# Performance work log

Measured on AMD Instinct MI355X. Metric: run time of the kernel, lower is better.

## Reference

```python
import jax, jax.numpy as jnp
import numpy as np

D_MODEL = 1024
NUM_HEAD = 16
D_K = D_MODEL // NUM_HEAD


def setup_inputs() -> dict:
    key = jax.random.key(0)
    ks = jax.random.split(key, 9)
    s = 1.0 / np.sqrt(D_MODEL)
    x = jax.random.normal(ks[0], (2, 2048, D_MODEL), dtype=jnp.float32)
    Wq = jax.random.uniform(ks[1], (D_MODEL, D_MODEL), jnp.float32, -s, s)
    bq = jax.random.uniform(ks[2], (D_MODEL,), jnp.float32, -s, s)
    Wk = jax.random.uniform(ks[3], (D_MODEL, D_MODEL), jnp.float32, -s, s)
    bk = jax.random.uniform(ks[4], (D_MODEL,), jnp.float32, -s, s)
    Wv = jax.random.uniform(ks[5], (D_MODEL, D_MODEL), jnp.float32, -s, s)
    bv = jax.random.uniform(ks[6], (D_MODEL,), jnp.float32, -s, s)
    Wo = jax.random.uniform(ks[7], (D_MODEL, D_MODEL), jnp.float32, -s, s)
    bo = jax.random.uniform(ks[8], (D_MODEL,), jnp.float32, -s, s)
    return {"x": x, "Wq": Wq, "bq": bq, "Wk": Wk, "bk": bk,
            "Wv": Wv, "bv": bv, "Wo": Wo, "bo": bo}


def reference(x, Wq, bq, Wk, bk, Wv, bv, Wo, bo):
    b, n, d = x.shape
    h, dk = NUM_HEAD, D_K
    # Linear projections (torch Linear: x @ W.T + b)
    q = (x @ Wq.T + bq).reshape(b, n, h, dk).transpose(0, 2, 1, 3)  # [b,h,n,dk]
    k = (x @ Wk.T + bk).reshape(b, n, h, dk).transpose(0, 2, 1, 3)
    v = (x @ Wv.T + bv).reshape(b, n, h, dk).transpose(0, 2, 1, 3)
    scores = jnp.einsum('bhqd,bhkd->bhqk', q, k) / jnp.sqrt(jnp.float32(dk))
    attn = jax.nn.softmax(scores, axis=-1)  # [b,h,n,n]
    out = jnp.einsum('bhqk,bhkd->bhqd', attn, v)
    out = out.transpose(0, 2, 1, 3).reshape(b, n, d)
    return out @ Wo.T + bo
```

## Files before the change

### kernel.cpp

```cpp
#include <hip/hip_runtime.h>

#define BATCH   2
#define SEQ     2048
#define DMODEL  1024
#define NHEAD   16
#define DKH     64
#define MTOT    (BATCH*SEQ)
#define KDIM    DMODEL

#define XB    0u
#define WQB   (4u*1024u*1024u)
#define WKB   (5u*1024u*1024u)
#define WVB   (6u*1024u*1024u)
#define WOB   (7u*1024u*1024u)
#define QOFF  (8u*1024u*1024u)
#define KOFF  (12u*1024u*1024u)
#define VOFF  (16u*1024u*1024u)
#define OOFF  (20u*1024u*1024u)

typedef __bf16 bf16x8 __attribute__((ext_vector_type(8)));
typedef __bf16 bf16x4 __attribute__((ext_vector_type(4)));
typedef float  f32x4  __attribute__((ext_vector_type(4)));
typedef float  f32x16 __attribute__((ext_vector_type(16)));

__device__ __forceinline__ void async16(const __bf16* g, __bf16* l) {
  __builtin_amdgcn_global_load_lds(
      (const __attribute__((address_space(1))) void*)g,
      (__attribute__((address_space(3))) void*)l, 16, 0, 0);
}

#define VWAIT(N) asm volatile("s_waitcnt vmcnt(" #N ")" ::: "memory")

__device__ __forceinline__ unsigned cvtpk_bf16(float lo, float hi) {
  unsigned r;
  asm("v_cvt_pk_bf16_f32 %0, %1, %2" : "=v"(r) : "v"(lo), "v"(hi));
  return r;
}
__device__ __forceinline__ void plswap(unsigned& a, unsigned& b) {
  asm("v_permlane32_swap_b32 %0, %1" : "+v"(a), "+v"(b));
}

__global__ __launch_bounds__(256) void cvt_fp32_bf16(
    const float* __restrict__ x,  const float* __restrict__ wq,
    const float* __restrict__ wk, const float* __restrict__ wv,
    const float* __restrict__ wo, __bf16* __restrict__ ws)
{
  const float* src; __bf16* dst; int n;
  switch (blockIdx.y) {
    case 0:  src = x;  dst = ws + XB;  n = 4 * 1024 * 1024; break;
    case 1:  src = wq; dst = ws + WQB; n = 1024 * 1024;     break;
    case 2:  src = wk; dst = ws + WKB; n = 1024 * 1024;     break;
    case 3:  src = wv; dst = ws + WVB; n = 1024 * 1024;     break;
    default: src = wo; dst = ws + WOB; n = 1024 * 1024;     break;
  }
  const int i = (blockIdx.x * 256 + threadIdx.x) * 8;
  if (i < n) {
    const float4 a = *(const float4*)(src + i);
    const float4 b = *(const float4*)(src + i + 4);
    bf16x8 o;
    o[0] = (__bf16)a.x; o[1] = (__bf16)a.y; o[2] = (__bf16)a.z; o[3] = (__bf16)a.w;
    o[4] = (__bf16)b.x; o[5] = (__bf16)b.y; o[6] = (__bf16)b.z; o[7] = (__bf16)b.w;
    *(bf16x8*)(dst + i) = o;
  }
}

__device__ __forceinline__ void gemm_stage128(
    const __bf16* __restrict__ A, const __bf16* __restrict__ W,
    int m0, int n0, int kt, __bf16* slot, int w, int lane)
{
#pragma unroll
  for (int issue = 0; issue < 2; ++issue) {
    const int cbase = issue * 256 + (w << 6);
    const int c     = cbase + lane;
    const int row   = c >> 2;
    const int goff  = ((c & 3) ^ (row & 3)) << 3;
    async16(A + (size_t)(m0 + row) * KDIM + kt + goff, slot + cbase * 8);
    async16(W + (size_t)(n0 + row) * KDIM + kt + goff, slot + 4096 + cbase * 8);
  }
}

__device__ __forceinline__ void gemm_step128(
    const __bf16* slot, int wr, int wc, int ln15, int quad, f32x4 (&acc)[4][4])
{
  const __bf16* A_lds = slot;
  const __bf16* B_lds = slot + 4096;
  bf16x8 af[4], bfr[4];
#pragma unroll
  for (int i = 0; i < 4; ++i) {
    const int row = wr + i * 16 + ln15;
    af[i] = *(const bf16x8*)&A_lds[row * 32 + ((quad ^ (row & 3)) << 3)];
  }
#pragma unroll
  for (int j = 0; j < 4; ++j) {
    const int row = wc + j * 16 + ln15;
    bfr[j] = *(const bf16x8*)&B_lds[row * 32 + ((quad ^ (row & 3)) << 3)];
  }
#pragma unroll
  for (int i = 0; i < 4; ++i)
#pragma unroll
    for (int j = 0; j < 4; ++j)
      acc[i][j] = __builtin_amdgcn_mfma_f32_16x16x32_bf16(af[i], bfr[j], acc[i][j], 0, 0, 0);
}

__device__ __forceinline__ void gemm128_core(
    const __bf16* __restrict__ A, const __bf16* __restrict__ W,
    int m0, int n0, __bf16* lds, f32x4 (&acc)[4][4])
{
  const int t    = threadIdx.x;
  const int w    = t >> 6;
  const int lane = t & 63;
  const int ln15 = lane & 15;
  const int quad = lane >> 4;
  const int wr   = (w >> 1) << 6;
  const int wc   = (w & 1) << 6;

#pragma unroll
  for (int i = 0; i < 4; ++i)
#pragma unroll
    for (int j = 0; j < 4; ++j) acc[i][j] = (f32x4){0.f, 0.f, 0.f, 0.f};

  __bf16* s0 = lds;
  __bf16* s1 = lds + 8192;
  __bf16* s2 = lds + 16384;

  gemm_stage128(A, W, m0, n0, 0,  s0, w, lane);
  gemm_stage128(A, W, m0, n0, 32, s1, w, lane);

  int kt = 0;
#pragma unroll 1
  for (int i3 = 0; i3 < 10; ++i3) {
    VWAIT(4); __builtin_amdgcn_s_barrier();
    gemm_stage128(A, W, m0, n0, kt + 64, s2, w, lane);
    gemm_step128(s0, wr, wc, ln15, quad, acc);

    VWAIT(4); __builtin_amdgcn_s_barrier();
    gemm_stage128(A, W, m0, n0, kt + 96, s0, w, lane);
    gemm_step128(s1, wr, wc, ln15, quad, acc);

    VWAIT(4); __builtin_amdgcn_s_barrier();
    gemm_stage128(A, W, m0, n0, kt + 128, s1, w, lane);
    gemm_step128(s2, wr, wc, ln15, quad, acc);
    kt += 96;
  }
  VWAIT(4); __builtin_amdgcn_s_barrier();
  gemm_step128(s0, wr, wc, ln15, quad, acc);
  VWAIT(0); __builtin_amdgcn_s_barrier();
  gemm_step128(s1, wr, wc, ln15, quad, acc);
}

__global__ __launch_bounds__(256) void qkv_gemm(
    const __bf16* __restrict__ X,
    const __bf16* __restrict__ Wq, const float* __restrict__ bq,
    const __bf16* __restrict__ Wk, const float* __restrict__ bk,
    const __bf16* __restrict__ Wv, const float* __restrict__ bv,
    __bf16* __restrict__ ws)
{
  __shared__ __align__(16) __bf16 lds[24576];

  const int z = blockIdx.z;
  const __bf16* W    = (z == 0) ? Wq : (z == 1) ? Wk : Wv;
  const float*  bias = (z == 0) ? bq : (z == 1) ? bk : bv;
  __bf16* out = ws + ((z == 0) ? QOFF : (z == 1) ? KOFF : VOFF);
  const float scale = (z == 0) ? 0.125f * 1.44269504088896f : 1.0f;

  const int m0 = blockIdx.x * 128;
  const int n0 = blockIdx.y * 128;

  f32x4 acc[4][4];
  gemm128_core(X, W, m0, n0, lds, acc);

  const int t = threadIdx.x, w = t >> 6, lane = t & 63;
  const int ln15 = lane & 15, quad = lane >> 4;
  const int wr = (w >> 1) << 6, wc = (w & 1) << 6;

  float bj4[4];
#pragma unroll
  for (int j = 0; j < 4; ++j) bj4[j] = bias[n0 + wc + j * 16 + ln15];

  __syncthreads();
  __bf16* scr = lds + (w << 10);

  const int bb = m0 >> 11;
  const int s_base = (m0 & 2047) + wr;
  const int h = (n0 + wc) >> 6;

  if (z != 2) {
    const int rdrow = lane & 15, rdseg = lane >> 4;
#pragma unroll
    for (int i = 0; i < 4; ++i) {
#pragma unroll
      for (int j = 0; j < 4; ++j)
#pragma unroll
        for (int rr = 0; rr < 4; ++rr)
          scr[(quad * 4 + rr) * 64 + j * 16 + ln15] =
              (__bf16)((acc[i][j][rr] + bj4[j]) * scale);
      bf16x8 v0 = *(const bf16x8*)&scr[rdrow * 64 + rdseg * 16];
      bf16x8 v1 = *(const bf16x8*)&scr[rdrow * 64 + rdseg * 16 + 8];
      const int s = s_base + i * 16 + rdrow;
      __bf16* p = out + (((size_t)(bb * NHEAD + h)) * SEQ + s) * DKH + rdseg * 16;
      *(bf16x8*)p = v0;
      *(bf16x8*)&p[8] = v1;
    }
  } else {
#pragma unroll
    for (int i = 0; i < 4; ++i) {
#pragma unroll
      for (int j = 0; j < 4; ++j) {
        bf16x4 pk;
#pragma unroll
        for (int rr = 0; rr < 4; ++rr) pk[rr] = (__bf16)(acc[i][j][rr] + bj4[j]);
        *(bf16x4*)&scr[(j * 16 + ln15) * 16 + quad * 4] = pk;
      }
      bf16x8 c0 = *(const bf16x8*)&scr[lane * 16];
      bf16x8 c1 = *(const bf16x8*)&scr[lane * 16 + 8];
      __bf16* p = out + (((size_t)(bb * NHEAD + h)) * DKH + lane) * SEQ
                      + s_base + i * 16;
      *(bf16x8*)p = c0;
      *(bf16x8*)&p[8] = c1;
    }
  }
}

__device__ __forceinline__ void out_stage(
    const __bf16* __restrict__ A, const __bf16* __restrict__ Wo,
    int m0, int n0, int kt, __bf16* slot, int w, int lane)
{
  {
    const int c = (w << 6) + lane;
    const int row = c >> 2;
    const int goff = ((c & 3) ^ (row & 3)) << 3;
    async16(A + (size_t)(m0 + row) * KDIM + kt + goff, slot + c * 8);
  }
#pragma unroll
  for (int issue = 0; issue < 2; ++issue) {
    const int cbase = issue * 256 + (w << 6);
    const int c = cbase + lane;
    const int row = c >> 2;
    const int goff = ((c & 3) ^ (row & 3)) << 3;
    async16(Wo + (size_t)(n0 + row) * KDIM + kt + goff, slot + 2048 + cbase * 8);
  }
}

__device__ __forceinline__ void out_step(
    const __bf16* slot, int w, int ln15, int quad, f32x4 (&acc)[4][2])
{
  const __bf16* A_lds = slot;
  const __bf16* B_lds = slot + 2048;
  bf16x8 af[4], bfr[2];
#pragma unroll
  for (int i = 0; i < 4; ++i) {
    const int row = i * 16 + ln15;
    af[i] = *(const bf16x8*)&A_lds[row * 32 + ((quad ^ (row & 3)) << 3)];
  }
#pragma unroll
  for (int j = 0; j < 2; ++j) {
    const int row = (w << 5) + j * 16 + ln15;
    bfr[j] = *(const bf16x8*)&B_lds[row * 32 + ((quad ^ (row & 3)) << 3)];
  }
#pragma unroll
  for (int i = 0; i < 4; ++i)
#pragma unroll
    for (int j = 0; j < 2; ++j)
      acc[i][j] = __builtin_amdgcn_mfma_f32_16x16x32_bf16(af[i], bfr[j], acc[i][j], 0, 0, 0);
}

__global__ __launch_bounds__(256) void out_gemm(
    const __bf16* __restrict__ A, const __bf16* __restrict__ Wo,
    const float* __restrict__ bo, float* __restrict__ out)
{
  __shared__ __align__(16) __bf16 lds[18432];

  const int m0 = blockIdx.x * 64;
  const int n0 = blockIdx.y * 128;

  const int t = threadIdx.x, w = t >> 6, lane = t & 63;
  const int ln15 = lane & 15, quad = lane >> 4;

  f32x4 acc[4][2];
#pragma unroll
  for (int i = 0; i < 4; ++i)
#pragma unroll
    for (int j = 0; j < 2; ++j) acc[i][j] = (f32x4){0.f, 0.f, 0.f, 0.f};

  __bf16* s0 = lds;
  __bf16* s1 = lds + 6144;
  __bf16* s2 = lds + 12288;

  out_stage(A, Wo, m0, n0, 0,  s0, w, lane);
  out_stage(A, Wo, m0, n0, 32, s1, w, lane);

  int kt = 0;
#pragma unroll 1
  for (int i3 = 0; i3 < 10; ++i3) {
    VWAIT(3); __builtin_amdgcn_s_barrier();
    out_stage(A, Wo, m0, n0, kt + 64, s2, w, lane);
    out_step(s0, w, ln15, quad, acc);

    VWAIT(3); __builtin_amdgcn_s_barrier();
    out_stage(A, Wo, m0, n0, kt + 96, s0, w, lane);
    out_step(s1, w, ln15, quad, acc);

    VWAIT(3); __builtin_amdgcn_s_barrier();
    out_stage(A, Wo, m0, n0, kt + 128, s1, w, lane);
    out_step(s2, w, ln15, quad, acc);
    kt += 96;
  }
  VWAIT(3); __builtin_amdgcn_s_barrier();
  out_step(s0, w, ln15, quad, acc);
  VWAIT(0); __builtin_amdgcn_s_barrier();
  out_step(s1, w, ln15, quad, acc);

  float bj2[2];
#pragma unroll
  for (int j = 0; j < 2; ++j) bj2[j] = bo[n0 + (w << 5) + j * 16 + ln15];

  __syncthreads();
  float* scrf = (float*)lds + (w << 9);

  const int rdrow = lane & 15, rdseg = lane >> 4;
#pragma unroll
  for (int i = 0; i < 4; ++i) {
#pragma unroll
    for (int j = 0; j < 2; ++j) {
      f32x4 v;
#pragma unroll
      for (int rr = 0; rr < 4; ++rr) v[rr] = acc[i][j][rr] + bj2[j];
      *(f32x4*)&scrf[(j * 16 + ln15) * 16 + quad * 4] = v;
    }
    const int m = m0 + i * 16 + rdrow;
    float* p = out + (size_t)m * DMODEL + n0 + (w << 5) + rdseg * 8;
#pragma unroll
    for (int cc = 0; cc < 2; ++cc) {
      f32x4 v;
#pragma unroll
      for (int e = 0; e < 4; ++e)
        v[e] = scrf[(rdseg * 8 + cc * 4 + e) * 16 + rdrow];
      *(f32x4*)&p[cc * 4] = v;
    }
  }
}

__device__ __forceinline__ void softmax_frag(const f32x16& s, float& l,
                                             bf16x8& pfa, bf16x8& pfb)
{
  float p[16];
#pragma unroll
  for (int r = 0; r < 16; ++r) {
    p[r] = __builtin_amdgcn_exp2f(s[r]);
    l += p[r];
  }
  unsigned A0 = cvtpk_bf16(p[0],  p[1]);
  unsigned A1 = cvtpk_bf16(p[2],  p[3]);
  unsigned B0 = cvtpk_bf16(p[4],  p[5]);
  unsigned B1 = cvtpk_bf16(p[6],  p[7]);
  unsigned C0 = cvtpk_bf16(p[8],  p[9]);
  unsigned C1 = cvtpk_bf16(p[10], p[11]);
  unsigned D0 = cvtpk_bf16(p[12], p[13]);
  unsigned D1 = cvtpk_bf16(p[14], p[15]);
  plswap(A0, B0);
  plswap(A1, B1);
  plswap(C0, D0);
  plswap(C1, D1);
  union { unsigned u[4]; bf16x8 v; } ua, ub;
  ua.u[0] = A0; ua.u[1] = A1; ua.u[2] = B0; ua.u[3] = B1;
  ub.u[0] = C0; ub.u[1] = C1; ub.u[2] = D0; ub.u[3] = D1;
  pfa = ua.v;
  pfb = ub.v;
}

__device__ __forceinline__ void pvstep(const __bf16* Vs, int kh, int KS, int hl,
                                       int ln31, const bf16x8& PF,
                                       f32x16& o0, f32x16& o1)
{
  const int vchunk = (kh << 3) + 2 * KS + hl;
  bf16x8 vf0 = *(const bf16x8*)&Vs[ln31 * 128 + ((vchunk ^ (ln31 & 15)) << 3)];
  bf16x8 vf1 = *(const bf16x8*)&Vs[(32 + ln31) * 128 +
                                   ((vchunk ^ ((32 + ln31) & 15)) << 3)];
  o0 = __builtin_amdgcn_mfma_f32_32x32x16_bf16(PF, vf0, o0, 0, 0, 0);
  o1 = __builtin_amdgcn_mfma_f32_32x32x16_bf16(PF, vf1, o1, 0, 0, 0);
}

__device__ __forceinline__ void attn_tile_compute(
    const __bf16* Ks, const __bf16* Vs, const bf16x8 (&qf)[4],
    int kh, int ln31, int hl, float& l_lane, f32x16& o0, f32x16& o1)
{
#pragma unroll
  for (int half = 0; half < 2; ++half) {
    f32x16 s;
#pragma unroll
    for (int r = 0; r < 16; ++r) s[r] = 0.f;
    const int kr = (kh << 6) + half * 32 + ln31;
    __builtin_amdgcn_s_setprio(1);
#pragma unroll
    for (int ks = 0; ks < 4; ++ks) {
      bf16x8 kf = *(const bf16x8*)&Ks[kr * 64 + (((2 * ks + hl) ^ (kr & 7)) << 3)];
      s = __builtin_amdgcn_mfma_f32_32x32x16_bf16(kf, qf[ks], s, 0, 0, 0);
    }
    __builtin_amdgcn_s_setprio(0);
    bf16x8 pa, pb;
    softmax_frag(s, l_lane, pa, pb);
    __builtin_amdgcn_s_setprio(1);
    pvstep(Vs, kh, half * 2 + 0, hl, ln31, pa, o0, o1);
    pvstep(Vs, kh, half * 2 + 1, hl, ln31, pb, o0, o1);
    __builtin_amdgcn_s_setprio(0);
  }
}

__global__ __launch_bounds__(512, 4) void attn_kernel(
    const __bf16* __restrict__ Qb, const __bf16* __restrict__ Kb,
    const __bf16* __restrict__ Vtb, __bf16* __restrict__ Ob)
{
  __shared__ __align__(16) __bf16 smem[5 * 128 * 64];
  __bf16* QP = smem;
  __bf16* K0 = smem + 8192;
  __bf16* V0 = smem + 16384;
  __bf16* K1 = smem + 24576;
  __bf16* V1 = smem + 32768;

  const int t = threadIdx.x, w = t >> 6, lane = t & 63;
  const int ln31 = lane & 31, hl = lane >> 5;
  const int g  = w & 3;
  const int kh = w >> 2;
  const int bh = blockIdx.x;
  const int q0 = blockIdx.y * 128;
  const int bb = bh >> 4, hh = bh & 15;

  const __bf16* Qg = Qb + (size_t)bh * SEQ * DKH + (size_t)q0 * DKH;
  const __bf16* Kg = Kb + (size_t)bh * SEQ * DKH;
  const __bf16* Vg = Vtb + (size_t)bh * DKH * SEQ;

  auto stage_kv = [&](int kt, __bf16* Ks, __bf16* Vs) {
#pragma unroll
    for (int issue = 0; issue < 2; ++issue) {
      const int cbase = issue * 512 + (w << 6);
      const int c = cbase + lane;
      const int krow = c >> 3;
      const int kgoff = ((c & 7) ^ (krow & 7)) << 3;
      async16(Kg + (size_t)(kt + krow) * DKH + kgoff, Ks + cbase * 8);
      const int vrow = c >> 4;
      const int vgoff = ((c & 15) ^ (vrow & 15)) << 3;
      async16(Vg + (size_t)vrow * SEQ + kt + vgoff, Vs + cbase * 8);
    }
  };

#pragma unroll
  for (int issue = 0; issue < 2; ++issue) {
    const int cbase = issue * 512 + (w << 6);
    const int c = cbase + lane;
    const int row = c >> 3;
    const int goff = ((c & 7) ^ (row & 7)) << 3;
    async16(Qg + (size_t)row * DKH + goff, QP + cbase * 8);
  }
  stage_kv(0, K0, V0);
  stage_kv(128, K1, V1);

  VWAIT(8);
  __builtin_amdgcn_s_barrier();

  const int qrow = (g << 5) + ln31;
  bf16x8 qf[4];
#pragma unroll
  for (int ks = 0; ks < 4; ++ks) {
    const int chunk = ((2 * ks + hl) ^ (qrow & 7));
    qf[ks] = *(const bf16x8*)&QP[qrow * 64 + (chunk << 3)];
  }

  float l_lane = 0.f;
  f32x16 o0, o1;
#pragma unroll
  for (int r = 0; r < 16; ++r) { o0[r] = 0.f; o1[r] = 0.f; }

#pragma unroll 1
  for (int j = 0; j < 14; j += 2) {
    VWAIT(4); __builtin_amdgcn_s_barrier();
    attn_tile_compute(K0, V0, qf, kh, ln31, hl, l_lane, o0, o1);
    __builtin_amdgcn_s_barrier();
    stage_kv((j + 2) * 128, K0, V0);

    VWAIT(4); __builtin_amdgcn_s_barrier();
    attn_tile_compute(K1, V1, qf, kh, ln31, hl, l_lane, o0, o1);
    __builtin_amdgcn_s_barrier();
    stage_kv((j + 3) * 128, K1, V1);
  }
  VWAIT(4); __builtin_amdgcn_s_barrier();
  attn_tile_compute(K0, V0, qf, kh, ln31, hl, l_lane, o0, o1);
  VWAIT(0); __builtin_amdgcn_s_barrier();
  attn_tile_compute(K1, V1, qf, kh, ln31, hl, l_lane, o0, o1);

  __syncthreads();
  float* cmb = (float*)smem;
  const int dsw = ln31 & 7;
  l_lane += __shfl_xor(l_lane, 32);

  if (w >= 4) {
    float* base = cmb + (g << 11);
#pragma unroll
    for (int gg = 0; gg < 4; ++gg) {
      const int qq = ((2 * gg + hl) ^ dsw) << 2;
      f32x4 va, vb;
#pragma unroll
      for (int rr = 0; rr < 4; ++rr) { va[rr] = o0[4 * gg + rr]; vb[rr] = o1[4 * gg + rr]; }
      *(f32x4*)&base[ln31 * 32 + qq]        = va;
      *(f32x4*)&base[(32 + ln31) * 32 + qq] = vb;
    }
    if (hl == 0) cmb[8192 + (g << 5) + ln31] = l_lane;
  }
  __syncthreads();
  if (w < 4) {
    float* base = cmb + (g << 11);
#pragma unroll
    for (int gg = 0; gg < 4; ++gg) {
      const int qq = ((2 * gg + hl) ^ dsw) << 2;
      const f32x4 va = *(const f32x4*)&base[ln31 * 32 + qq];
      const f32x4 vb = *(const f32x4*)&base[(32 + ln31) * 32 + qq];
#pragma unroll
      for (int rr = 0; rr < 4; ++rr) { o0[4 * gg + rr] += va[rr]; o1[4 * gg + rr] += vb[rr]; }
    }
    const float inv = 1.0f / (l_lane + cmb[8192 + (g << 5) + ln31]);

#pragma unroll
    for (int r = 0; r < 16; ++r) {
      const int qi = (r & 3) + 8 * (r >> 2) + 4 * hl;
      const float iq = __shfl(inv, qi);
      const int q = q0 + (g << 5) + qi;
      __bf16* rowp = Ob + ((size_t)(bb * SEQ + q)) * DMODEL + hh * DKH;
      rowp[ln31]      = (__bf16)(o0[r] * iq);
      rowp[32 + ln31] = (__bf16)(o1[r] * iq);
    }
  }
}

extern "C" void kernel_launch(void* const* d_in, const int* in_sizes, int n_in,
                              void* d_out, int out_size, void* d_ws, size_t ws_size,
                              hipStream_t stream)
{
  const float* x  = (const float*)d_in[0];
  const float* Wq = (const float*)d_in[1];
  const float* bq = (const float*)d_in[2];
  const float* Wk = (const float*)d_in[3];
  const float* bk = (const float*)d_in[4];
  const float* Wv = (const float*)d_in[5];
  const float* bv = (const float*)d_in[6];
  const float* Wo = (const float*)d_in[7];
  const float* bo = (const float*)d_in[8];
  float*  out = (float*)d_out;
  __bf16* ws  = (__bf16*)d_ws;

  cvt_fp32_bf16<<<dim3(2048, 5, 1), 256, 0, stream>>>(x, Wq, Wk, Wv, Wo, ws);

  qkv_gemm<<<dim3(MTOT / 128, DMODEL / 128, 3), 256, 0, stream>>>(
      ws + XB, ws + WQB, bq, ws + WKB, bk, ws + WVB, bv, ws);

  attn_kernel<<<dim3(BATCH * NHEAD, SEQ / 128), 512, 0, stream>>>(
      ws + QOFF, ws + KOFF, ws + VOFF, ws + OOFF);

  out_gemm<<<dim3(MTOT / 64, DMODEL / 128), 256, 0, stream>>>(
      ws + OOFF, ws + WOB, bo, out);
}
```

Before: 182.9 us.

## Split QKV GEMM 128x128 tile across 8 waves instead of 4

The QKV projection kernel now launches 512 threads per block, with each wave computing a 64x32 sub-tile instead of 64x64. Staging loads are spread over all threads with one async load per operand, and the epilogue writes narrower per-wave slices. The aim is more waves per CU to hide memory and MFMA latency, at the cost of lower register-level reuse per wave and more barrier participants.

Result: no change. 180.6 us (median of 2 runs) (-1.3%).

```diff
diff --git a/kernel.cpp b/kernel.cpp
--- a/kernel.cpp
+++ b/kernel.cpp
@@ -64,91 +64,41 @@
   }
 }
 
-__device__ __forceinline__ void gemm_stage128(
+__device__ __forceinline__ void qkv_stage(
     const __bf16* __restrict__ A, const __bf16* __restrict__ W,
-    int m0, int n0, int kt, __bf16* slot, int w, int lane)
-{
-#pragma unroll
-  for (int issue = 0; issue < 2; ++issue) {
-    const int cbase = issue * 256 + (w << 6);
-    const int c     = cbase + lane;
-    const int row   = c >> 2;
-    const int goff  = ((c & 3) ^ (row & 3)) << 3;
-    async16(A + (size_t)(m0 + row) * KDIM + kt + goff, slot + cbase * 8);
-    async16(W + (size_t)(n0 + row) * KDIM + kt + goff, slot + 4096 + cbase * 8);
-  }
-}
-
-__device__ __forceinline__ void gemm_step128(
-    const __bf16* slot, int wr, int wc, int ln15, int quad, f32x4 (&acc)[4][4])
+    int m0, int n0, int kt, __bf16* slot, int t)
+{
+  const int c    = t;
+  const int row  = c >> 2;
+  const int goff = ((c & 3) ^ (row & 3)) << 3;
+  async16(A + (size_t)(m0 + row) * KDIM + kt + goff, slot + c * 8);
+  async16(W + (size_t)(n0 + row) * KDIM + kt + goff, slot + 4096 + c * 8);
+}
+
+__device__ __forceinline__ void qkv_step(
+    const __bf16* slot, int wr, int wc, int ln15, int quad, f32x4 (&acc)[4][2])
 {
   const __bf16* A_lds = slot;
   const __bf16* B_lds = slot + 4096;
-  bf16x8 af[4], bfr[4];
+  bf16x8 af[4], bfr[2];
 #pragma unroll
   for (int i = 0; i < 4; ++i) {
     const int row = wr + i * 16 + ln15;
     af[i] = *(const bf16x8*)&A_lds[row * 32 + ((quad ^ (row & 3)) << 3)];
   }
 #pragma unroll
-  for (int j = 0; j < 4; ++j) {
+  for (int j = 0; j < 2; ++j) {
     const int row = wc + j * 16 + ln15;
     bfr[j] = *(const bf16x8*)&B_lds[row * 32 + ((quad ^ (row & 3)) << 3)];
   }
 #pragma unroll
   for (int i = 0; i < 4; ++i)
 #pragma unroll
-    for (int j = 0; j < 4; ++j)
+    for (int j = 0; j < 2; ++j)
       acc[i][j] = __builtin_amdgcn_mfma_f32_16x16x32_bf16(af[i], bfr[j], acc[i][j], 0, 0, 0);
 }
 
-__device__ __forceinline__ void gemm128_core(
-    const __bf16* __restrict__ A, const __bf16* __restrict__ W,
-    int m0, int n0, __bf16* lds, f32x4 (&acc)[4][4])
-{
-  const int t    = threadIdx.x;
-  const int w    = t >> 6;
-  const int lane = t & 63;
-  const int ln15 = lane & 15;
-  const int quad = lane >> 4;
-  const int wr   = (w >> 1) << 6;
-  const int wc   = (w & 1) << 6;
-
-#pragma unroll
-  for (int i = 0; i < 4; ++i)
-#pragma unroll
-    for (int j = 0; j < 4; ++j) acc[i][j] = (f32x4){0.f, 0.f, 0.f, 0.f};
-
-  __bf16* s0 = lds;
-  __bf16* s1 = lds + 8192;
-  __bf16* s2 = lds + 16384;
-
-  gemm_stage128(A, W, m0, n0, 0,  s0, w, lane);
-  gemm_stage128(A, W, m0, n0, 32, s1, w, lane);
-
-  int kt = 0;
-#pragma unroll 1
-  for (int i3 = 0; i3 < 10; ++i3) {
-    VWAIT(4); __builtin_amdgcn_s_barrier();
-    gemm_stage128(A, W, m0, n0, kt + 64, s2, w, lane);
-    gemm_step128(s0, wr, wc, ln15, quad, acc);
-
-    VWAIT(4); __builtin_amdgcn_s_barrier();
-    gemm_stage128(A, W, m0, n0, kt + 96, s0, w, lane);
-    gemm_step128(s1, wr, wc, ln15, quad, acc);
-
-    VWAIT(4); __builtin_amdgcn_s_barrier();
-    gemm_stage128(A, W, m0, n0, kt + 128, s1, w, lane);
-    gemm_step128(s2, wr, wc, ln15, quad, acc);
-    kt += 96;
-  }
-  VWAIT(4); __builtin_amdgcn_s_barrier();
-  gemm_step128(s0, wr, wc, ln15, quad, acc);
-  VWAIT(0); __builtin_amdgcn_s_barrier();
-  gemm_step128(s1, wr, wc, ln15, quad, acc);
-}
-
-__global__ __launch_bounds__(256) void qkv_gemm(
+__global__ __launch_bounds__(512, 3) void qkv_gemm(
     const __bf16* __restrict__ X,
     const __bf16* __restrict__ Wq, const float* __restrict__ bq,
     const __bf16* __restrict__ Wk, const float* __restrict__ bk,
@@ -166,16 +116,48 @@
   const int m0 = blockIdx.x * 128;
   const int n0 = blockIdx.y * 128;
 
-  f32x4 acc[4][4];
-  gemm128_core(X, W, m0, n0, lds, acc);
-
   const int t = threadIdx.x, w = t >> 6, lane = t & 63;
   const int ln15 = lane & 15, quad = lane >> 4;
-  const int wr = (w >> 1) << 6, wc = (w & 1) << 6;
-
-  float bj4[4];
-#pragma unroll
-  for (int j = 0; j < 4; ++j) bj4[j] = bias[n0 + wc + j * 16 + ln15];
+  const int wr = (w >> 2) << 6;
+  const int wc = (w & 3) << 5;
+
+  f32x4 acc[4][2];
+#pragma unroll
+  for (int i = 0; i < 4; ++i)
+#pragma unroll
+    for (int j = 0; j < 2; ++j) acc[i][j] = (f32x4){0.f, 0.f, 0.f, 0.f};
+
+  __bf16* s0 = lds;
+  __bf16* s1 = lds + 8192;
+  __bf16* s2 = lds + 16384;
+
+  qkv_stage(X, W, m0, n0, 0,  s0, t);
+  qkv_stage(X, W, m0, n0, 32, s1, t);
+
+  int kt = 0;
+#pragma unroll 1
+  for (int i3 = 0; i3 < 10; ++i3) {
+    VWAIT(2); __builtin_amdgcn_s_barrier();
+    qkv_stage(X, W, m0, n0, kt + 64, s2, t);
+    qkv_step(s0, wr, wc, ln15, quad, acc);
+
+    VWAIT(2); __builtin_amdgcn_s_barrier();
+    qkv_stage(X, W, m0, n0, kt + 96, s0, t);
+    qkv_step(s1, wr, wc, ln15, quad, acc);
+
+    VWAIT(2); __builtin_amdgcn_s_barrier();
+    qkv_stage(X, W, m0, n0, kt + 128, s1, t);
+    qkv_step(s2, wr, wc, ln15, quad, acc);
+    kt += 96;
+  }
+  VWAIT(2); __builtin_amdgcn_s_barrier();
+  qkv_step(s0, wr, wc, ln15, quad, acc);
+  VWAIT(0); __builtin_amdgcn_s_barrier();
+  qkv_step(s1, wr, wc, ln15, quad, acc);
+
+  float bj2[2];
+#pragma unroll
+  for (int j = 0; j < 2; ++j) bj2[j] = bias[n0 + wc + j * 16 + ln15];
 
   __syncthreads();
   __bf16* scr = lds + (w << 10);
@@ -189,34 +171,32 @@
 #pragma unroll
     for (int i = 0; i < 4; ++i) {
 #pragma unroll
-      for (int j = 0; j < 4; ++j)
+      for (int j = 0; j < 2; ++j)
 #pragma unroll
         for (int rr = 0; rr < 4; ++rr)
-          scr[(quad * 4 + rr) * 64 + j * 16 + ln15] =
-              (__bf16)((acc[i][j][rr] + bj4[j]) * scale);
-      bf16x8 v0 = *(const bf16x8*)&scr[rdrow * 64 + rdseg * 16];
-      bf16x8 v1 = *(const bf16x8*)&scr[rdrow * 64 + rdseg * 16 + 8];
+          scr[(quad * 4 + rr) * 32 + j * 16 + ln15] =
+              (__bf16)((acc[i][j][rr] + bj2[j]) * scale);
+      bf16x8 v = *(const bf16x8*)&scr[rdrow * 32 + rdseg * 8];
       const int s = s_base + i * 16 + rdrow;
-      __bf16* p = out + (((size_t)(bb * NHEAD + h)) * SEQ + s) * DKH + rdseg * 16;
-      *(bf16x8*)p = v0;
-      *(bf16x8*)&p[8] = v1;
+      __bf16* p = out + (((size_t)(bb * NHEAD + h)) * SEQ + s) * DKH
+                      + (wc & 63) + rdseg * 8;
+      *(bf16x8*)p = v;
     }
   } else {
 #pragma unroll
     for (int i = 0; i < 4; ++i) {
 #pragma unroll
-      for (int j = 0; j < 4; ++j) {
+      for (int j = 0; j < 2; ++j) {
         bf16x4 pk;
 #pragma unroll
-        for (int rr = 0; rr < 4; ++rr) pk[rr] = (__bf16)(acc[i][j][rr] + bj4[j]);
+        for (int rr = 0; rr < 4; ++rr) pk[rr] = (__bf16)(acc[i][j][rr] + bj2[j]);
         *(bf16x4*)&scr[(j * 16 + ln15) * 16 + quad * 4] = pk;
       }
-      bf16x8 c0 = *(const bf16x8*)&scr[lane * 16];
-      bf16x8 c1 = *(const bf16x8*)&scr[lane * 16 + 8];
-      __bf16* p = out + (((size_t)(bb * NHEAD + h)) * DKH + lane) * SEQ
-                      + s_base + i * 16;
+      const int dloc = lane >> 1, half = lane & 1;
+      bf16x8 c0 = *(const bf16x8*)&scr[dloc * 16 + half * 8];
+      __bf16* p = out + (((size_t)(bb * NHEAD + h)) * DKH + (wc & 63) + dloc) * SEQ
+                      + s_base + i * 16 + half * 8;
       *(bf16x8*)p = c0;
-      *(bf16x8*)&p[8] = c1;
     }
   }
 }
@@ -548,7 +528,7 @@
 
   cvt_fp32_bf16<<<dim3(2048, 5, 1), 256, 0, stream>>>(x, Wq, Wk, Wv, Wo, ws);
 
-  qkv_gemm<<<dim3(MTOT / 128, DMODEL / 128, 3), 256, 0, stream>>>(
+  qkv_gemm<<<dim3(MTOT / 128, DMODEL / 128, 3), 512, 0, stream>>>(
       ws + XB, ws + WQB, bq, ws + WKB, bk, ws + WVB, bv, ws);
 
   attn_kernel<<<dim3(BATCH * NHEAD, SEQ / 128), 512, 0, stream>>>(
```
